# Kernel tuning notes

Hardware: AMD Instinct MI355X
Metric: run time of the kernel (lower is better)

The kernel has to match this reference:

```python
import jax, jax.numpy as jnp
import numpy as np
from math import comb

G, NPG, D = 32, 128, 128   # graphs, nodes-per-graph, hidden dim
N = G * NPG                # 4096 nodes per side
E = 65536                  # edges per side (avg degree 16)
K = 6                      # Bernstein order (bern_k)
S, DCONV, DTR = 16, 4, 8   # mamba d_state, d_conv, dt_rank
HE = 27
SIGMAS = [1.0, 10.0, 100.0, 1000.0, 10000.0]


def _leaky(x, s=0.02):
    return jnp.where(x >= 0, x, s * x)


def _bnorm(x, g, b, eps=1e-5):
    m = jnp.mean(x, axis=0)
    v = jnp.var(x, axis=0)
    return (x - m) * jax.lax.rsqrt(v + eps) * g + b


def _bern_prop(x, src, dst, w, temp):
    # BernNet Bern_prop: Bernstein polynomial of sym-normalized Laplacian with weights relu(temp)
    n = x.shape[0]
    temp = jax.nn.relu(temp)
    deg = jax.ops.segment_sum(w, src, num_segments=n)
    dinv = jnp.where(deg > 0, 1.0 / jnp.sqrt(deg + 1e-12), 0.0)
    nw = (w * dinv[src] * dinv[dst])[:, None]
    adj = lambda v: jax.ops.segment_sum(nw * v[src], dst, num_segments=n)
    tmps = [x]
    xv = x
    for _ in range(K):
        xv = xv + adj(xv)          # (2I - L) v = v + A_norm v
        tmps.append(xv)
    out = (comb(K, 0) / 2 ** K) * temp[0] * tmps[K]
    for i in range(K):
        v = tmps[K - i - 1]
        for _ in range(i + 1):
            v = v - adj(v)         # L v = v - A_norm v
        out = out + (comb(K, i + 1) / 2 ** K) * temp[i + 1] * v
    return out


def _mamba(h, in_w, conv_w, conv_b, xproj_w, dt_w, dt_b, A_log, Dp, out_w):
    # Mamba block, d_model=D, expand=1 (d_inner=D), d_state=S, d_conv=DCONV
    Bb, L, _ = h.shape
    xq, z = jnp.split(h @ in_w, 2, axis=-1)             # [B,L,D] each
    xp = jnp.pad(xq, ((0, 0), (DCONV - 1, 0), (0, 0)))  # causal depthwise conv
    xc = conv_b + sum(xp[:, k:k + L, :] * conv_w[:, k] for k in range(DCONV))
    xc = jax.nn.silu(xc)
    dbl = xc @ xproj_w                                  # [B,L,DTR+2S]
    dt = jax.nn.softplus(dbl[..., :DTR] @ dt_w + dt_b)  # [B,L,D]
    Bm = dbl[..., DTR:DTR + S]
    Cm = dbl[..., DTR + S:]
    A = -jnp.exp(A_log)                                 # [D,S]
    dA = jnp.exp(dt[..., None] * A)                     # [B,L,D,S]
    dBx = dt[..., None] * Bm[:, :, None, :] * xc[..., None]

    def step(hs, ins):
        dA_t, dBx_t, C_t = ins
        hs = dA_t * hs + dBx_t
        return hs, jnp.einsum('bds,bs->bd', hs, C_t)

    h0 = jnp.zeros((Bb, D, S), h.dtype)
    _, ys = jax.lax.scan(step, h0, (jnp.swapaxes(dA, 0, 1),
                                    jnp.swapaxes(dBx, 0, 1),
                                    jnp.swapaxes(Cm, 0, 1)))
    y = jnp.swapaxes(ys, 0, 1) + xc * Dp
    return (y * jax.nn.silu(z)) @ out_w


def _xattn(q, k, v, mask):
    a = mask * (q @ k.T) - 1000.0 * (1.0 - mask)
    return jax.nn.softmax(a, axis=1) @ v


def setup_inputs():
    key = jax.random.key(0)
    ks = jax.random.split(key, 32)
    f = jnp.float32
    nrm = lambda k, shp, sc=1.0: jax.random.normal(k, shp, dtype=f) * sc
    h_lig = nrm(ks[0], (N, D), 0.5)
    h_rec = nrm(ks[1], (N, D), 0.5)
    x_lig = nrm(ks[2], (N, 3))
    x_rec = nrm(ks[3], (N, 3))
    he_1 = jax.random.uniform(ks[4], (E, HE), dtype=f)
    he_2 = jax.random.uniform(ks[5], (E, HE), dtype=f)
    g = (jnp.arange(E) // (E // G)).astype(jnp.int32)
    src1 = g * NPG + jax.random.randint(ks[6], (E,), 0, NPG, dtype=jnp.int32)
    dst1 = g * NPG + jax.random.randint(ks[7], (E,), 0, NPG, dtype=jnp.int32)
    src2 = g * NPG + jax.random.randint(ks[8], (E,), 0, NPG, dtype=jnp.int32)
    dst2 = g * NPG + jax.random.randint(ks[9], (E,), 0, NPG, dtype=jnp.int32)
    edge_index_1 = jnp.stack([src1, dst1])
    edge_index_2 = jnp.stack([src2, dst2])
    batch = (jnp.arange(N) // NPG).astype(jnp.int32)
    rng = np.random.default_rng(0)
    def mkperm(src):
        # lexsort([deg + noise, batch]) with batch as primary key
        deg = np.bincount(np.asarray(src), minlength=N).astype(np.float32)
        return jnp.asarray(np.lexsort((deg + rng.random(N).astype(np.float32),
                                       np.asarray(batch))).astype(np.int32))
    perm_1 = mkperm(src1)
    perm_2 = mkperm(src2)
    p = {}
    p['emlp_w1'] = nrm(ks[10], (32, D), 0.1)
    p['emlp_b1'] = jnp.zeros((D,), f)
    p['emlp_bn_g'] = jnp.ones((D,), f)
    p['emlp_bn_b'] = jnp.zeros((D,), f)
    p['emlp_w2'] = nrm(ks[11], (D, 1), 0.1)
    p['emlp_b2'] = jnp.zeros((1,), f)
    p['bern_temp'] = jnp.ones((K + 1,), f)
    p['m_in_w'] = nrm(ks[12], (D, 2 * D), 0.05)
    p['m_conv_w'] = nrm(ks[13], (D, DCONV), 0.2)
    p['m_conv_b'] = jnp.zeros((D,), f)
    p['m_xproj_w'] = nrm(ks[14], (D, DTR + 2 * S), 0.05)
    p['m_dt_w'] = nrm(ks[15], (DTR, D), 0.2)
    p['m_dt_b'] = jnp.full((D,), -4.0, f)
    p['m_A_log'] = jnp.log(jnp.broadcast_to(jnp.arange(1, S + 1, dtype=f), (D, S)))
    p['m_D'] = jnp.ones((D,), f)
    p['m_out_w'] = nrm(ks[16], (D, D), 0.05)
    p['q_w'] = nrm(ks[17], (D, D), 0.05)
    p['k_w'] = nrm(ks[18], (D, D), 0.05)
    p['v_w'] = nrm(ks[19], (D, D), 0.05)
    p['bn1_g'] = jnp.ones((D,), f)
    p['bn1_b'] = jnp.zeros((D,), f)
    p['bn2_g'] = jnp.ones((D,), f)
    p['bn2_b'] = jnp.zeros((D,), f)
    p['ff_w1'] = nrm(ks[20], (D, 2 * D), 0.05)
    p['ff_b1'] = jnp.zeros((2 * D,), f)
    p['ff_w2'] = nrm(ks[21], (2 * D, D), 0.05)
    p['ff_b2'] = jnp.zeros((D,), f)
    return dict(h_lig=h_lig, h_rec=h_rec, x_lig=x_lig, x_rec=x_rec,
                he_1=he_1, he_2=he_2, **p,
                edge_index_1=edge_index_1, edge_index_2=edge_index_2,
                batch_1=batch, batch_2=batch, perm_1=perm_1, perm_2=perm_2)


def reference(h_lig, h_rec, x_lig, x_rec, he_1, he_2,
              emlp_w1, emlp_b1, emlp_bn_g, emlp_bn_b, emlp_w2, emlp_b2,
              bern_temp, m_in_w, m_conv_w, m_conv_b, m_xproj_w, m_dt_w,
              m_dt_b, m_A_log, m_D, m_out_w, q_w, k_w, v_w,
              bn1_g, bn1_b, bn2_g, bn2_b, ff_w1, ff_b1, ff_w2, ff_b2,
              edge_index_1, edge_index_2, batch_1, batch_2, perm_1, perm_2):

    def side(h, x, he, ei, perm):
        src, dst = ei[0], ei[1]
        d2 = jnp.sum((x[src] - x[dst]) ** 2, axis=1, keepdims=True)
        ew = jnp.concatenate([jnp.exp(-d2 / s) for s in SIGMAS], axis=1)  # [E,5]
        t = _leaky(jnp.concatenate([ew, he], axis=1) @ emlp_w1 + emlp_b1)
        t = _bnorm(t, emlp_bn_g, emlp_bn_b)
        w = jax.nn.relu(t @ emlp_w2 + emlp_b2)[:, 0]                      # [E]
        h_local = _bern_prop(h, src, dst, w, bern_temp)
        inv = jnp.argsort(perm)
        hd = h[perm].reshape(G, NPG, D)   # uniform graph sizes -> exact dense batch
        ha = _mamba(hd, m_in_w, m_conv_w, m_conv_b, m_xproj_w, m_dt_w,
                    m_dt_b, m_A_log, m_D, m_out_w).reshape(N, D)[inv]
        return _bnorm(h + h_local + ha, bn1_g, bn1_b)

    hl = side(h_lig, x_lig, he_1, edge_index_1, perm_1)
    hr = side(h_rec, x_rec, he_2, edge_index_2, perm_2)
    mask = (batch_1[:, None] == batch_2[None, :]).astype(hl.dtype)
    cl = _xattn(_leaky(hl @ q_w), _leaky(hr @ k_w), hr @ v_w, mask)
    cr = _xattn(_leaky(hr @ q_w), _leaky(hl @ k_w), hl @ v_w, mask.T)
    hl = hl + cl
    hr = hr + cr
    ff = lambda h: jax.nn.relu(h @ ff_w1 + ff_b1) @ ff_w2 + ff_b2
    hl = _bnorm(hl + ff(hl), bn2_g, bn2_b)
    hr = _bnorm(hr + ff(hr), bn2_g, bn2_b)
    return hl, hr
```

## Files before the change

kernel.cpp:

```cpp
#include <hip/hip_runtime.h>
#include <math.h>

#define G_    32
#define NPG_  128
#define D_    128
#define N_    4096
#define E_    65536
#define ND_   (N_*D_)

#define W_OFF     0
#define DEG_OFF   65536
#define STATS_OFF 69632
#define BUF0      71680
#define HL_OFF    (BUF0 + 0*ND_)
#define HA_OFF    (BUF0 + 1*ND_)
#define X1_OFF    (BUF0 + 2*ND_)
#define HMID_OFF  (BUF0 + 3*ND_)
#define XC_OFF    (BUF0 + 4*ND_)
#define DTB_OFF   (BUF0 + 5*ND_)
#define YB_OFF    (BUF0 + 6*ND_)
#define XZ_OFF    (BUF0 + 7*ND_)
#define DBL_OFF   (BUF0 + 9*ND_)
#define SS_       ((size_t)(DBL_OFF + N_*40))

__device__ __forceinline__ float leakyf(float x){ return x >= 0.f ? x : 0.02f*x; }
__device__ __forceinline__ float siluf (float x){ return x / (1.f + expf(-x)); }

__device__ __forceinline__ void edge_feat(const float* __restrict__ x,
                                          const float* __restrict__ he,
                                          const int* __restrict__ ei,
                                          int e, float* feat, int& sN, int& dN)
{
  sN = ei[e]; dN = ei[E_ + e];
  float dx = x[sN*3+0]-x[dN*3+0];
  float dy = x[sN*3+1]-x[dN*3+1];
  float dz = x[sN*3+2]-x[dN*3+2];
  float d2 = dx*dx + dy*dy + dz*dz;
  feat[0] = expf(-d2/1.f);
  feat[1] = expf(-d2/10.f);
  feat[2] = expf(-d2/100.f);
  feat[3] = expf(-d2/1000.f);
  feat[4] = expf(-d2/10000.f);
#pragma unroll
  for (int j = 0; j < 27; ++j) feat[5+j] = he[(size_t)e*27 + j];
}

__global__ __launch_bounds__(256)
void edge_stats_kernel(const float* __restrict__ xl, const float* __restrict__ xr,
                       const float* __restrict__ hel, const float* __restrict__ her,
                       const int* __restrict__ ei1, const int* __restrict__ ei2,
                       const float* __restrict__ w1, const float* __restrict__ b1,
                       float* __restrict__ ws)
{
  int side = blockIdx.y;
  const float* x  = side ? xr  : xl;
  const float* he = side ? her : hel;
  const int*   ei = side ? ei2 : ei1;
  float* stats = ws + (size_t)side*SS_ + STATS_OFF;
  __shared__ float featl[256*36];
  __shared__ float csum[2][128], cssq[2][128];
  int tid = threadIdx.x;
  {
    int sN, dN; float feat[32];
    edge_feat(x, he, ei, blockIdx.x*256 + tid, feat, sN, dN);
#pragma unroll
    for (int j4 = 0; j4 < 8; ++j4)
      *(float4*)&featl[tid*36 + j4*4] = *(float4*)&feat[j4*4];
  }
  int c = tid & 127, hh = tid >> 7;
  float w1c[32];
#pragma unroll
  for (int j = 0; j < 32; ++j) w1c[j] = w1[j*128 + c];
  float b1c = b1[c];
  __syncthreads();
  float s1 = 0.f, s2 = 0.f;
  for (int e = 0; e < 128; ++e) {
    const float* f = &featl[(hh*128 + e)*36];
    float acc = b1c;
#pragma unroll
    for (int j4 = 0; j4 < 8; ++j4) {
      float4 f4 = *(const float4*)&f[j4*4];
      acc += f4.x*w1c[j4*4] + f4.y*w1c[j4*4+1] + f4.z*w1c[j4*4+2] + f4.w*w1c[j4*4+3];
    }
    float t = leakyf(acc);
    s1 += t; s2 += t*t;
  }
  csum[hh][c] = s1; cssq[hh][c] = s2;
  __syncthreads();
  if (tid < 128) {
    atomicAdd(&stats[tid],     csum[0][tid] + csum[1][tid]);
    atomicAdd(&stats[128+tid], cssq[0][tid] + cssq[1][tid]);
  }
}

__global__ void edge_finalize_kernel(const float* __restrict__ g_, const float* __restrict__ b_,
                                     const float* __restrict__ w2, const float* __restrict__ b2,
                                     float* __restrict__ ws)
{
  int side = blockIdx.y;
  float* stats = ws + (size_t)side*SS_ + STATS_OFF;
  __shared__ float red[128];
  int c = threadIdx.x;
  const float invE = 1.f/(float)E_;
  float mean = stats[c]*invE;
  float var  = fmaxf(stats[128+c]*invE - mean*mean, 0.f);
  float scale = rsqrtf(var + 1e-5f) * g_[c];
  stats[256+c] = scale * w2[c];
  red[c] = (b_[c] - mean*scale) * w2[c];
  __syncthreads();
  for (int off = 64; off; off >>= 1) { if (c < off) red[c] += red[c+off]; __syncthreads(); }
  if (c == 0) stats[384] = red[0] + b2[0];
}

__global__ __launch_bounds__(256)
void edge_w_kernel(const float* __restrict__ xl, const float* __restrict__ xr,
                   const float* __restrict__ hel, const float* __restrict__ her,
                   const int* __restrict__ ei1, const int* __restrict__ ei2,
                   const float* __restrict__ w1, const float* __restrict__ b1,
                   float* __restrict__ ws)
{
  int side = blockIdx.y;
  const float* x  = side ? xr  : xl;
  const float* he = side ? her : hel;
  const int*   ei = side ? ei2 : ei1;
  float* base = ws + (size_t)side*SS_;
  const float* stats = base + STATS_OFF;
  float* wbuf = base + W_OFF;
  float* deg  = base + DEG_OFF;
  __shared__ float w1t[128*32];
  __shared__ float b1l[128], all_[128];
  int tid = threadIdx.x;
  for (int i = tid; i < 4096; i += 256) {
    int j = i & 31, c = i >> 5;
    w1t[c*32 + j] = w1[j*128 + c];
  }
  if (tid < 128) { b1l[tid] = b1[tid]; all_[tid] = stats[256+tid]; }
  __syncthreads();
  int e = blockIdx.x*256 + tid;
  int sN, dN; float feat[32];
  edge_feat(x, he, ei, e, feat, sN, dN);
  float accw = stats[384];
  for (int c = 0; c < 128; ++c) {
    float acc = b1l[c];
#pragma unroll
    for (int j4 = 0; j4 < 8; ++j4) {
      float4 w4 = *(const float4*)&w1t[c*32 + j4*4];
      acc += feat[j4*4]*w4.x + feat[j4*4+1]*w4.y + feat[j4*4+2]*w4.z + feat[j4*4+3]*w4.w;
    }
    accw += leakyf(acc)*all_[c];
  }
  float w = fmaxf(accw, 0.f);
  wbuf[e] = w;
  atomicAdd(&deg[sN], w);
}

__global__ __launch_bounds__(256)
void bern_horner_kernel(const float* __restrict__ hl_in, const float* __restrict__ hr_in,
                        const int* __restrict__ ei1, const int* __restrict__ ei2,
                        const float* __restrict__ bern_temp, float* __restrict__ ws)
{
  int side = blockIdx.y;
  int g  = blockIdx.x >> 2;
  int d0 = (blockIdx.x & 3) * 32;
  const float* h  = side ? hr_in : hl_in;
  const int*   ei = side ? ei2 : ei1;
  float* base = ws + (size_t)side*SS_;
  const float* wbuf = base + W_OFF;
  const float* deg  = base + DEG_OFF;
  float* hloc = base + HL_OFF;

  __shared__ float A[128*132];
  __shared__ float v[128*32];
  int tid = threadIdx.x;
  for (int i = tid; i < 128*132; i += 256) A[i] = 0.f;

  const float btab[7][7] = {
    { 1,  6, 15,  20, 15,  6,  1},
    { 1,  4,  5,   0, -5, -4, -1},
    { 1,  2, -1,  -4, -1,  2,  1},
    { 1,  0, -3,   0,  3,  0, -1},
    { 1, -2, -1,   4, -1, -2,  1},
    { 1, -4,  5,   0, -5,  4, -1},
    { 1, -6, 15, -20, 15, -6,  1}};
  const float comb6[7] = {1,6,15,20,15,6,1};
  float a[7];
#pragma unroll
  for (int m = 0; m < 7; ++m) a[m] = 0.f;
#pragma unroll
  for (int j = 0; j < 7; ++j) {
    float tj = fmaxf(bern_temp[j], 0.f) * comb6[j] * (1.f/64.f);
#pragma unroll
    for (int m = 0; m < 7; ++m) a[m] += tj * btab[j][m];
  }
  __syncthreads();

  int ebase = g*2048, nbase = g*128;
  for (int i = tid; i < 2048; i += 256) {
    int e = ebase + i;
    int sN = ei[e], dN = ei[E_ + e];
    float ds_ = deg[sN], dd_ = deg[dN];
    float aa = ds_ > 0.f ? rsqrtf(ds_ + 1e-12f) : 0.f;
    float bb = dd_ > 0.f ? rsqrtf(dd_ + 1e-12f) : 0.f;
    atomicAdd(&A[(dN - nbase)*132 + (sN - nbase)], wbuf[e]*aa*bb);
  }

  const int db = (tid & 7)*4;
  const int rb = (tid >> 3)*4;
  float hreg[4][4], r[4][4], t[4][4];
#pragma unroll
  for (int i = 0; i < 4; ++i) {
    float4 h4 = *(const float4*)&h[(size_t)(nbase + rb + i)*128 + d0 + db];
    hreg[i][0]=h4.x; hreg[i][1]=h4.y; hreg[i][2]=h4.z; hreg[i][3]=h4.w;
#pragma unroll
    for (int jj = 0; jj < 4; ++jj) r[i][jj] = a[6]*hreg[i][jj];
  }

  for (int step = 5; step >= 0; --step) {
    __syncthreads();
#pragma unroll
    for (int i = 0; i < 4; ++i)
      *(float4*)&v[(rb+i)*32 + db] = make_float4(r[i][0], r[i][1], r[i][2], r[i][3]);
    __syncthreads();
#pragma unroll
    for (int i = 0; i < 4; ++i)
#pragma unroll
      for (int jj = 0; jj < 4; ++jj) t[i][jj] = 0.f;
    for (int k = 0; k < 128; k += 4) {
      float4 V0 = *(const float4*)&v[(k+0)*32 + db];
      float4 V1 = *(const float4*)&v[(k+1)*32 + db];
      float4 V2 = *(const float4*)&v[(k+2)*32 + db];
      float4 V3 = *(const float4*)&v[(k+3)*32 + db];
#pragma unroll
      for (int i = 0; i < 4; ++i) {
        float4 A4 = *(const float4*)&A[(rb+i)*132 + k];
        t[i][0] += A4.x*V0.x + A4.y*V1.x + A4.z*V2.x + A4.w*V3.x;
        t[i][1] += A4.x*V0.y + A4.y*V1.y + A4.z*V2.y + A4.w*V3.y;
        t[i][2] += A4.x*V0.z + A4.y*V1.z + A4.z*V2.z + A4.w*V3.z;
        t[i][3] += A4.x*V0.w + A4.y*V1.w + A4.z*V2.w + A4.w*V3.w;
      }
    }
    float ak = a[step];
#pragma unroll
    for (int i = 0; i < 4; ++i)
#pragma unroll
      for (int jj = 0; jj < 4; ++jj) r[i][jj] = t[i][jj] + ak*hreg[i][jj];
  }

#pragma unroll
  for (int i = 0; i < 4; ++i)
    *(float4*)&hloc[(size_t)(nbase + rb + i)*128 + d0 + db] =
        make_float4(r[i][0], r[i][1], r[i][2], r[i][3]);
}

template<int K, int NC, int TC, int CSPLIT, int ACT, int GATHER, int SCATTER, int ADDC, int BIAS>
__global__ __launch_bounds__(256)
void gemm_kernel(const float* __restrict__ A0, const float* __restrict__ A1, int lda,
                 const float* __restrict__ W, const float* __restrict__ bias,
                 float* __restrict__ C0, float* __restrict__ C1, int ldc,
                 const int* __restrict__ idx0, const int* __restrict__ idx1,
                 const float* __restrict__ add0, const float* __restrict__ add1)
{
  int side = blockIdx.y;
  const float* A = side ? A1 : A0;
  float* C = side ? C1 : C0;
  const int* idx = side ? idx1 : idx0;
  const float* addsrc = side ? add1 : add0;
  constexpr int RPT = TC/8;
  constexpr int CLEN = NC/CSPLIT;
  __shared__ float Alds[32][K];
  __shared__ float Wlds[K][TC];
  const int tid = threadIdx.x;
  const int r0 = (blockIdx.x / CSPLIT) * 32;
  const int cbase = (blockIdx.x % CSPLIT) * CLEN;
  for (int i = tid*4; i < 32*K; i += 1024) {
    int r = i / K, k = i % K;
    int row = GATHER ? idx[r0 + r] : (r0 + r);
    *(float4*)&Alds[r][k] = *(const float4*)&A[(size_t)row*lda + k];
  }
  for (int c0 = cbase; c0 < cbase + CLEN; c0 += TC) {
    __syncthreads();
    for (int i = tid*4; i < K*TC; i += 1024) {
      int k = i / TC, c = i % TC;
      if (c0 + c < NC) *(float4*)&Wlds[k][c] = *(const float4*)&W[k*NC + c0 + c];
      else             *(float4*)&Wlds[k][c] = make_float4(0.f,0.f,0.f,0.f);
    }
    __syncthreads();
    const int cl = tid % TC;
    const int rsub = (tid / TC) * RPT;
    float accv[RPT];
#pragma unroll
    for (int j = 0; j < RPT; ++j) accv[j] = 0.f;
    for (int k = 0; k < K; k += 4) {
      float w0 = Wlds[k][cl], w1v = Wlds[k+1][cl], w2v = Wlds[k+2][cl], w3v = Wlds[k+3][cl];
#pragma unroll
      for (int j = 0; j < RPT; ++j) {
        float4 a4 = *(const float4*)&Alds[rsub+j][k];
        accv[j] += a4.x*w0 + a4.y*w1v + a4.z*w2v + a4.w*w3v;
      }
    }
    int c = c0 + cl;
    if (c < NC) {
#pragma unroll
      for (int j = 0; j < RPT; ++j) {
        int row  = r0 + rsub + j;
        int orow = SCATTER ? idx[row] : row;
        float vv = accv[j];
        if (BIAS)     vv += bias[c];
        if (ACT == 1) vv = leakyf(vv);
        if (ACT == 2) vv = fmaxf(vv, 0.f);
        if (ADDC)     vv += addsrc[(size_t)orow*ldc + c];
        C[(size_t)orow*ldc + c] = vv;
      }
    }
  }
}

__global__ __launch_bounds__(256)
void qkv_kernel(const float* __restrict__ qw, const float* __restrict__ kw,
                const float* __restrict__ vw, float* __restrict__ ws)
{
  int side = blockIdx.y;
  int mat  = blockIdx.z;
  float* base = ws + (size_t)side*SS_;
  const float* A = base + HMID_OFF;
  const float* W = mat == 0 ? qw : (mat == 1 ? kw : vw);
  float* C = base + (mat == 0 ? XC_OFF : (mat == 1 ? DTB_OFF : YB_OFF));
  __shared__ float Alds[32][128];
  __shared__ float Wlds[128][64];
  const int tid = threadIdx.x;
  const int r0 = (blockIdx.x >> 1) * 32;
  const int c0 = (blockIdx.x & 1) * 64;
  for (int i = tid*4; i < 32*128; i += 1024)
    *(float4*)&Alds[i>>7][i&127] = *(const float4*)&A[(size_t)(r0 + (i>>7))*128 + (i&127)];
  for (int i = tid*4; i < 128*64; i += 1024)
    *(float4*)&Wlds[i>>6][i&63] = *(const float4*)&W[(i>>6)*128 + c0 + (i&63)];
  __syncthreads();
  const int cl = tid & 63;
  const int rsub = (tid >> 6) * 8;
  float accv[8];
#pragma unroll
  for (int j = 0; j < 8; ++j) accv[j] = 0.f;
  for (int k = 0; k < 128; k += 4) {
    float w0 = Wlds[k][cl], w1v = Wlds[k+1][cl], w2v = Wlds[k+2][cl], w3v = Wlds[k+3][cl];
#pragma unroll
    for (int j = 0; j < 8; ++j) {
      float4 a4 = *(const float4*)&Alds[rsub+j][k];
      accv[j] += a4.x*w0 + a4.y*w1v + a4.z*w2v + a4.w*w3v;
    }
  }
#pragma unroll
  for (int j = 0; j < 8; ++j) {
    float vv = accv[j];
    if (mat < 2) vv = leakyf(vv);
    C[(size_t)(r0 + rsub + j)*128 + c0 + cl] = vv;
  }
}

__global__ __launch_bounds__(256)
void conv_kernel(const float* __restrict__ cw, const float* __restrict__ cb, float* __restrict__ ws)
{
  int side = blockIdx.y;
  float* base = ws + (size_t)side*SS_;
  const float* xz = base + XZ_OFF;
  float* xc = base + XC_OFF;
  int i = blockIdx.x*256 + threadIdx.x;
  int j = i >> 7, d = i & 127;
  int l = j & 127;
  float a = cb[d];
#pragma unroll
  for (int k = 0; k < 4; ++k) {
    int ll = l - 3 + k;
    if (ll >= 0) a += xz[(size_t)(j-3+k)*256 + d] * cw[d*4 + k];
  }
  xc[i] = siluf(a);
}

__global__ __launch_bounds__(256)
void scan_kernel(const float* __restrict__ A_log, const float* __restrict__ Dp,
                 const float* __restrict__ dtw, const float* __restrict__ dtbias,
                 float* __restrict__ ws)
{
  int side = blockIdx.z;
  int g  = blockIdx.x;
  int d0 = blockIdx.y * 16;
  float* base = ws + (size_t)side*SS_;
  const float* dbl = base + DBL_OFF;
  const float* xcb = base + XC_OFF;
  float* xz = base + XZ_OFF;

  __shared__ float ldbl[128][40];
  __shared__ float lxc[128][16];
  __shared__ float ldt[128][16];
  __shared__ float lz[128][16];
  __shared__ float ly[128][16];
  __shared__ float ltw[8][16];
  __shared__ float ltb[16];

  int tid = threadIdx.x;
  int rowbase = g*128;
  if (tid < 128)      ltw[tid>>4][tid&15] = dtw[(tid>>4)*128 + d0 + (tid&15)];
  else if (tid < 144) ltb[tid-128] = dtbias[d0 + (tid-128)];
  for (int i = tid; i < 128*40; i += 256)
    ((float*)ldbl)[i] = dbl[(size_t)rowbase*40 + i];
  for (int i = tid; i < 2048; i += 256) {
    int l = i >> 4, dd = i & 15;
    lxc[l][dd] = xcb[(size_t)(rowbase+l)*128 + d0 + dd];
    lz[l][dd]  = xz[(size_t)(rowbase+l)*256 + 128 + d0 + dd];
  }
  __syncthreads();
  for (int i = tid; i < 2048; i += 256) {
    int l = i >> 4, dd = i & 15;
    float a = ltb[dd];
#pragma unroll
    for (int k = 0; k < 8; ++k) a += ldbl[l][k]*ltw[k][dd];
    ldt[l][dd] = a > 20.f ? a : log1pf(expf(a));
  }
  __syncthreads();

  int s = tid & 15, dl = (tid >> 4) & 15;
  float Ac  = -expf(A_log[(d0+dl)*16 + s]);
  float dpv = Dp[d0+dl];
  float hsv = 0.f;
  for (int l = 0; l < 128; ++l) {
    float dtv = ldt[l][dl];
    float xcv = lxc[l][dl];
    float Bv  = ldbl[l][8+s];
    float Cv  = ldbl[l][24+s];
    hsv = expf(dtv*Ac)*hsv + (dtv*xcv)*Bv;
    float val = hsv*Cv;
    val += __shfl_xor(val, 1, 16);
    val += __shfl_xor(val, 2, 16);
    val += __shfl_xor(val, 4, 16);
    val += __shfl_xor(val, 8, 16);
    if (s == 0) ly[l][dl] = val + xcv*dpv;
  }
  __syncthreads();
  for (int i = tid; i < 2048; i += 256) {
    int l = i >> 4, dd = i & 15;
    float y = ly[l][dd];
    float z = lz[l][dd];
    xz[(size_t)(rowbase+l)*256 + d0 + dd] = y * siluf(z);
  }
}

__global__ __launch_bounds__(256)
void stats_kernel(const float* __restrict__ hl_in, const float* __restrict__ hr_in,
                  float* __restrict__ ws, int mode, int statsoff)
{
  int side = blockIdx.y;
  float* base = ws + (size_t)side*SS_;
  const float* h    = side ? hr_in : hl_in;
  const float* hloc = base + HL_OFF;
  const float* ha   = base + HA_OFF;
  float* x1 = base + X1_OFF;
  float* stats = base + STATS_OFF + statsoff;
  int tid = threadIdx.x;
  int c = tid & 127;
  float s1 = 0.f, s2 = 0.f;
  for (int it = 0; it < 16; ++it) {
    int r = blockIdx.x*32 + (tid >> 7) + it*2;
    size_t i = (size_t)r*128 + c;
    float v;
    if (mode == 0) { v = h[i] + hloc[i] + ha[i]; x1[i] = v; }
    else           { v = ha[i]; }
    s1 += v; s2 += v*v;
  }
  __shared__ float red[256];
  red[tid] = s1; __syncthreads();
  if (tid < 128) atomicAdd(&stats[tid], red[tid] + red[tid+128]);
  __syncthreads();
  red[tid] = s2; __syncthreads();
  if (tid < 128) atomicAdd(&stats[128+tid], red[tid] + red[tid+128]);
}

__global__ void bn_finalize_kernel(const float* __restrict__ g_, const float* __restrict__ b_,
                                   float* __restrict__ ws, int statsoff, float invM)
{
  int side = blockIdx.y;
  float* stats = ws + (size_t)side*SS_ + STATS_OFF + statsoff;
  int c = threadIdx.x;
  float mean = stats[c]*invM;
  float var  = fmaxf(stats[128+c]*invM - mean*mean, 0.f);
  float scale = rsqrtf(var + 1e-5f) * g_[c];
  stats[256+c] = scale;
  stats[384+c] = b_[c] - mean*scale;
}

__global__ __launch_bounds__(256)
void bn_apply_kernel(float* __restrict__ ws, float* __restrict__ dout,
                     int srcoff, int dstoff, int statsoff, int to_dout)
{
  int side = blockIdx.y;
  float* base = ws + (size_t)side*SS_;
  const float* src = base + srcoff;
  const float* stats = base + STATS_OFF + statsoff;
  float* dst = to_dout ? (dout + (size_t)side*ND_) : (base + dstoff);
  size_t i = (size_t)blockIdx.x*256 + threadIdx.x;
  int c = (int)(i & 127);
  dst[i] = src[i]*stats[256+c] + stats[384+c];
}

__global__ __launch_bounds__(256)
void attn_kernel(float* __restrict__ ws)
{
  int dir = blockIdx.z;
  int g   = blockIdx.x;
  int rt  = blockIdx.y;
  float* baseq = ws + (size_t)dir*SS_;
  float* basek = ws + (size_t)(1-dir)*SS_;
  const float* qb = baseq + XC_OFF;
  const float* kb = basek + DTB_OFF;
  const float* vb = basek + YB_OFF;
  const float* hm = baseq + HMID_OFF;
  float* h2 = baseq + X1_OFF;

  __shared__ float KT[128][132];
  __shared__ float Qs[32][132];
  __shared__ float sp[32][132];

  const int tid = threadIdx.x;
  const int cl  = tid & 31;
  const int r0  = (tid >> 5) * 4;
  const int c0  = cl * 4;
  const int rowg = g*128 + rt*32;

  {
    const float* qsrc = qb + (size_t)rowg*128;
    for (int i = tid; i < 32*32; i += 256) {
      int r = i >> 5, d4 = i & 31;
      *(float4*)&Qs[r][d4*4] = *(const float4*)&qsrc[(size_t)r*128 + d4*4];
    }
  }
  {
    const float* ksrc = kb + (size_t)(g*128)*128;
    for (int i = tid; i < 128*32; i += 256) {
      int d4 = i >> 7, n = i & 127;
      float4 k4 = *(const float4*)&ksrc[(size_t)n*128 + d4*4];
      KT[d4*4+0][n] = k4.x;
      KT[d4*4+1][n] = k4.y;
      KT[d4*4+2][n] = k4.z;
      KT[d4*4+3][n] = k4.w;
    }
  }
  __syncthreads();

  float acc[4][4];
#pragma unroll
  for (int i = 0; i < 4; ++i)
#pragma unroll
    for (int j = 0; j < 4; ++j) acc[i][j] = 0.f;

  for (int d = 0; d < 128; d += 4) {
    float4 k0 = *(const float4*)&KT[d+0][c0];
    float4 k1 = *(const float4*)&KT[d+1][c0];
    float4 k2 = *(const float4*)&KT[d+2][c0];
    float4 k3 = *(const float4*)&KT[d+3][c0];
#pragma unroll
    for (int i = 0; i < 4; ++i) {
      float4 q4 = *(const float4*)&Qs[r0+i][d];
      acc[i][0] += q4.x*k0.x + q4.y*k1.x + q4.z*k2.x + q4.w*k3.x;
      acc[i][1] += q4.x*k0.y + q4.y*k1.y + q4.z*k2.y + q4.w*k3.y;
      acc[i][2] += q4.x*k0.z + q4.y*k1.z + q4.z*k2.z + q4.w*k3.z;
      acc[i][3] += q4.x*k0.w + q4.y*k1.w + q4.z*k2.w + q4.w*k3.w;
    }
  }

  float inv[4];
#pragma unroll
  for (int i = 0; i < 4; ++i) {
    float m = fmaxf(fmaxf(acc[i][0], acc[i][1]), fmaxf(acc[i][2], acc[i][3]));
#pragma unroll
    for (int off = 1; off < 32; off <<= 1) m = fmaxf(m, __shfl_xor(m, off, 32));
    float p0 = expf(acc[i][0]-m), p1 = expf(acc[i][1]-m);
    float p2 = expf(acc[i][2]-m), p3 = expf(acc[i][3]-m);
    float s = p0 + p1 + p2 + p3;
#pragma unroll
    for (int off = 1; off < 32; off <<= 1) s += __shfl_xor(s, off, 32);
    inv[i] = 1.f/s;
    *(float4*)&sp[r0+i][c0] = make_float4(p0, p1, p2, p3);
  }
  __syncthreads();

  {
    const float* vsrc = vb + (size_t)(g*128)*128;
    for (int i = tid; i < 128*32; i += 256) {
      int n = i >> 5, d4 = i & 31;
      *(float4*)&KT[n][d4*4] = *(const float4*)&vsrc[(size_t)n*128 + d4*4];
    }
  }
  __syncthreads();

  float o[4][4];
#pragma unroll
  for (int i = 0; i < 4; ++i)
#pragma unroll
    for (int j = 0; j < 4; ++j) o[i][j] = 0.f;

  for (int n = 0; n < 128; n += 4) {
    float4 v0 = *(const float4*)&KT[n+0][c0];
    float4 v1 = *(const float4*)&KT[n+1][c0];
    float4 v2 = *(const float4*)&KT[n+2][c0];
    float4 v3 = *(const float4*)&KT[n+3][c0];
#pragma unroll
    for (int i = 0; i < 4; ++i) {
      float4 p4 = *(const float4*)&sp[r0+i][n];
      o[i][0] += p4.x*v0.x + p4.y*v1.x + p4.z*v2.x + p4.w*v3.x;
      o[i][1] += p4.x*v0.y + p4.y*v1.y + p4.z*v2.y + p4.w*v3.y;
      o[i][2] += p4.x*v0.z + p4.y*v1.z + p4.z*v2.z + p4.w*v3.z;
      o[i][3] += p4.x*v0.w + p4.y*v1.w + p4.z*v2.w + p4.w*v3.w;
    }
  }

#pragma unroll
  for (int i = 0; i < 4; ++i) {
    size_t off = (size_t)(rowg + r0 + i)*128 + c0;
    float4 hm4 = *(const float4*)&hm[off];
    float4 r4;
    r4.x = hm4.x + o[i][0]*inv[i];
    r4.y = hm4.y + o[i][1]*inv[i];
    r4.z = hm4.z + o[i][2]*inv[i];
    r4.w = hm4.w + o[i][3]*inv[i];
    *(float4*)&h2[off] = r4;
  }
}

extern "C" void kernel_launch(void* const* d_in, const int* in_sizes, int n_in,
                              void* d_out, int out_size, void* d_ws, size_t ws_size,
                              hipStream_t stream)
{
  const float* h_lig     = (const float*)d_in[0];
  const float* h_rec     = (const float*)d_in[1];
  const float* x_lig     = (const float*)d_in[2];
  const float* x_rec     = (const float*)d_in[3];
  const float* he_1      = (const float*)d_in[4];
  const float* he_2      = (const float*)d_in[5];
  const float* emlp_w1   = (const float*)d_in[6];
  const float* emlp_b1   = (const float*)d_in[7];
  const float* emlp_bn_g = (const float*)d_in[8];
  const float* emlp_bn_b = (const float*)d_in[9];
  const float* emlp_w2   = (const float*)d_in[10];
  const float* emlp_b2   = (const float*)d_in[11];
  const float* bern_temp = (const float*)d_in[12];
  const float* m_in_w    = (const float*)d_in[13];
  const float* m_conv_w  = (const float*)d_in[14];
  const float* m_conv_b  = (const float*)d_in[15];
  const float* m_xproj_w = (const float*)d_in[16];
  const float* m_dt_w    = (const float*)d_in[17];
  const float* m_dt_b    = (const float*)d_in[18];
  const float* m_A_log   = (const float*)d_in[19];
  const float* m_D       = (const float*)d_in[20];
  const float* m_out_w   = (const float*)d_in[21];
  const float* q_w       = (const float*)d_in[22];
  const float* k_w       = (const float*)d_in[23];
  const float* v_w       = (const float*)d_in[24];
  const float* bn1_g     = (const float*)d_in[25];
  const float* bn1_b     = (const float*)d_in[26];
  const float* bn2_g     = (const float*)d_in[27];
  const float* bn2_b     = (const float*)d_in[28];
  const float* ff_w1     = (const float*)d_in[29];
  const float* ff_b1     = (const float*)d_in[30];
  const float* ff_w2     = (const float*)d_in[31];
  const float* ff_b2     = (const float*)d_in[32];
  const int*   ei1       = (const int*)d_in[33];
  const int*   ei2       = (const int*)d_in[34];
  const int*   perm1     = (const int*)d_in[37];
  const int*   perm2     = (const int*)d_in[38];

  float* ws   = (float*)d_ws;
  float* dout = (float*)d_out;

#define B0(off) (ws + (size_t)(off))
#define B1(off) (ws + SS_ + (size_t)(off))

  for (int s = 0; s < 2; ++s)
    hipMemsetAsync((char*)d_ws + ((size_t)s*SS_ + DEG_OFF)*sizeof(float), 0,
                   (N_ + 2048)*sizeof(float), stream);

  edge_stats_kernel<<<dim3(256,2), 256, 0, stream>>>(x_lig,x_rec,he_1,he_2,ei1,ei2,emlp_w1,emlp_b1,ws);
  edge_finalize_kernel<<<dim3(1,2), 128, 0, stream>>>(emlp_bn_g,emlp_bn_b,emlp_w2,emlp_b2,ws);
  edge_w_kernel<<<dim3(256,2), 256, 0, stream>>>(x_lig,x_rec,he_1,he_2,ei1,ei2,emlp_w1,emlp_b1,ws);

  bern_horner_kernel<<<dim3(G_*4,2), 256, 0, stream>>>(h_lig,h_rec,ei1,ei2,bern_temp,ws);

  gemm_kernel<128,256,64,4,0,1,0,0,0><<<dim3(512,2),256,0,stream>>>(
      h_lig,h_rec,128, m_in_w,nullptr, B0(XZ_OFF),B1(XZ_OFF),256, perm1,perm2, nullptr,nullptr);
  conv_kernel<<<dim3(2048,2), 256, 0, stream>>>(m_conv_w,m_conv_b,ws);
  gemm_kernel<128,40,64,1,0,0,0,0,0><<<dim3(128,2),256,0,stream>>>(
      B0(XC_OFF),B1(XC_OFF),128, m_xproj_w,nullptr, B0(DBL_OFF),B1(DBL_OFF),40, nullptr,nullptr, nullptr,nullptr);
  scan_kernel<<<dim3(32,8,2), 256, 0, stream>>>(m_A_log,m_D,m_dt_w,m_dt_b,ws);
  gemm_kernel<128,128,64,2,0,0,1,0,0><<<dim3(256,2),256,0,stream>>>(
      B0(XZ_OFF),B1(XZ_OFF),256, m_out_w,nullptr, B0(HA_OFF),B1(HA_OFF),128, perm1,perm2, nullptr,nullptr);

  stats_kernel<<<dim3(128,2), 256, 0, stream>>>(h_lig,h_rec,ws,0,512);
  bn_finalize_kernel<<<dim3(1,2), 128, 0, stream>>>(bn1_g,bn1_b,ws,512,1.f/(float)N_);
  bn_apply_kernel<<<dim3(2048,2), 256, 0, stream>>>(ws,dout,X1_OFF,HMID_OFF,512,0);

  qkv_kernel<<<dim3(256,2,3), 256, 0, stream>>>(q_w,k_w,v_w,ws);
  attn_kernel<<<dim3(32,4,2), 256, 0, stream>>>(ws);

  gemm_kernel<128,256,64,4,2,0,0,0,1><<<dim3(512,2),256,0,stream>>>(
      B0(X1_OFF),B1(X1_OFF),128, ff_w1,ff_b1, B0(XZ_OFF),B1(XZ_OFF),256, nullptr,nullptr, nullptr,nullptr);
  gemm_kernel<256,128,32,4,0,0,0,1,1><<<dim3(512,2),256,0,stream>>>(
      B0(XZ_OFF),B1(XZ_OFF),256, ff_w2,ff_b2, B0(HA_OFF),B1(HA_OFF),128, nullptr,nullptr, B0(X1_OFF),B1(X1_OFF));
  stats_kernel<<<dim3(128,2), 256, 0, stream>>>(h_lig,h_rec,ws,1,1024);
  bn_finalize_kernel<<<dim3(1,2), 128, 0, stream>>>(bn2_g,bn2_b,ws,1024,1.f/(float)N_);
  bn_apply_kernel<<<dim3(2048,2), 256, 0, stream>>>(ws,dout,HA_OFF,0,1024,1);
}
```

Baseline: 458.1 us.

## Precompute transposed edge-MLP weights once and restructure edge stats per-thread

A small kernel now writes a transposed copy of the edge-MLP first-layer weights into workspace once, and both edge kernels read it directly instead of each block re-transposing into shared memory. The stats kernel changes from a shared-memory feature tile with a column-per-thread loop to a row-per-thread loop. Column sums and sums of squares are reduced with wavefront shuffles and then atomically added per wave. The exp divisions become multiplications by reciprocal constants. This trades shared-memory staging and per-block transposes for uniform global/scalar weight loads, at the cost of many shuffles per channel and more atomics (one set per wave instead of per block).

```diff
diff --git a/kernel.cpp b/kernel.cpp
--- a/kernel.cpp
+++ b/kernel.cpp
@@ -21,7 +21,8 @@
 #define YB_OFF    (BUF0 + 6*ND_)
 #define XZ_OFF    (BUF0 + 7*ND_)
 #define DBL_OFF   (BUF0 + 9*ND_)
-#define SS_       ((size_t)(DBL_OFF + N_*40))
+#define WT_OFF    (DBL_OFF + N_*40)
+#define SS_       ((size_t)(WT_OFF + 4096))
 
 __device__ __forceinline__ float leakyf(float x){ return x >= 0.f ? x : 0.02f*x; }
 __device__ __forceinline__ float siluf (float x){ return x / (1.f + expf(-x)); }
@@ -36,20 +37,28 @@
   float dy = x[sN*3+1]-x[dN*3+1];
   float dz = x[sN*3+2]-x[dN*3+2];
   float d2 = dx*dx + dy*dy + dz*dz;
-  feat[0] = expf(-d2/1.f);
-  feat[1] = expf(-d2/10.f);
-  feat[2] = expf(-d2/100.f);
-  feat[3] = expf(-d2/1000.f);
-  feat[4] = expf(-d2/10000.f);
+  feat[0] = expf(-d2);
+  feat[1] = expf(d2 * -0.1f);
+  feat[2] = expf(d2 * -0.01f);
+  feat[3] = expf(d2 * -0.001f);
+  feat[4] = expf(d2 * -0.0001f);
 #pragma unroll
   for (int j = 0; j < 27; ++j) feat[5+j] = he[(size_t)e*27 + j];
+}
+
+__global__ void wt_kernel(const float* __restrict__ w1, float* __restrict__ wt)
+{
+  for (int k = threadIdx.x; k < 4096; k += 256) {
+    int c = k >> 5, j = k & 31;
+    wt[k] = w1[j*128 + c];
+  }
 }
 
 __global__ __launch_bounds__(256)
 void edge_stats_kernel(const float* __restrict__ xl, const float* __restrict__ xr,
                        const float* __restrict__ hel, const float* __restrict__ her,
                        const int* __restrict__ ei1, const int* __restrict__ ei2,
-                       const float* __restrict__ w1, const float* __restrict__ b1,
+                       const float* __restrict__ wt, const float* __restrict__ b1,
                        float* __restrict__ ws)
 {
   int side = blockIdx.y;
@@ -57,40 +66,37 @@
   const float* he = side ? her : hel;
   const int*   ei = side ? ei2 : ei1;
   float* stats = ws + (size_t)side*SS_ + STATS_OFF;
-  __shared__ float featl[256*36];
-  __shared__ float csum[2][128], cssq[2][128];
   int tid = threadIdx.x;
-  {
-    int sN, dN; float feat[32];
-    edge_feat(x, he, ei, blockIdx.x*256 + tid, feat, sN, dN);
-#pragma unroll
-    for (int j4 = 0; j4 < 8; ++j4)
-      *(float4*)&featl[tid*36 + j4*4] = *(float4*)&feat[j4*4];
-  }
-  int c = tid & 127, hh = tid >> 7;
-  float w1c[32];
-#pragma unroll
-  for (int j = 0; j < 32; ++j) w1c[j] = w1[j*128 + c];
-  float b1c = b1[c];
-  __syncthreads();
-  float s1 = 0.f, s2 = 0.f;
-  for (int e = 0; e < 128; ++e) {
-    const float* f = &featl[(hh*128 + e)*36];
-    float acc = b1c;
-#pragma unroll
-    for (int j4 = 0; j4 < 8; ++j4) {
-      float4 f4 = *(const float4*)&f[j4*4];
-      acc += f4.x*w1c[j4*4] + f4.y*w1c[j4*4+1] + f4.z*w1c[j4*4+2] + f4.w*w1c[j4*4+3];
-    }
-    float t = leakyf(acc);
-    s1 += t; s2 += t*t;
-  }
-  csum[hh][c] = s1; cssq[hh][c] = s2;
-  __syncthreads();
-  if (tid < 128) {
-    atomicAdd(&stats[tid],     csum[0][tid] + csum[1][tid]);
-    atomicAdd(&stats[128+tid], cssq[0][tid] + cssq[1][tid]);
-  }
+  int lane = tid & 63;
+  int sN, dN; float feat[32];
+  edge_feat(x, he, ei, blockIdx.x*256 + tid, feat, sN, dN);
+  float kA1 = 0.f, kA2 = 0.f, kB1 = 0.f, kB2 = 0.f;
+  for (int c = 0; c < 128; ++c) {
+    const float* wc = &wt[c*32];
+    float a0 = 0.f, a1 = 0.f, a2 = 0.f, a3 = 0.f;
+#pragma unroll
+    for (int j = 0; j < 32; j += 4) {
+      a0 += feat[j+0]*wc[j+0];
+      a1 += feat[j+1]*wc[j+1];
+      a2 += feat[j+2]*wc[j+2];
+      a3 += feat[j+3]*wc[j+3];
+    }
+    float t = leakyf(b1[c] + ((a0+a1) + (a2+a3)));
+    float s1 = t, s2 = t*t;
+#pragma unroll
+    for (int off = 1; off < 64; off <<= 1) {
+      s1 += __shfl_xor(s1, off, 64);
+      s2 += __shfl_xor(s2, off, 64);
+    }
+    if ((c & 63) == lane) {
+      if (c < 64) { kA1 = s1; kA2 = s2; }
+      else        { kB1 = s1; kB2 = s2; }
+    }
+  }
+  atomicAdd(&stats[lane],          kA1);
+  atomicAdd(&stats[128 + lane],    kA2);
+  atomicAdd(&stats[64 + lane],     kB1);
+  atomicAdd(&stats[128 + 64 + lane], kB2);
 }
 
 __global__ void edge_finalize_kernel(const float* __restrict__ g_, const float* __restrict__ b_,
@@ -116,7 +122,7 @@
 void edge_w_kernel(const float* __restrict__ xl, const float* __restrict__ xr,
                    const float* __restrict__ hel, const float* __restrict__ her,
                    const int* __restrict__ ei1, const int* __restrict__ ei2,
-                   const float* __restrict__ w1, const float* __restrict__ b1,
+                   const float* __restrict__ wt, const float* __restrict__ b1,
                    float* __restrict__ ws)
 {
   int side = blockIdx.y;
@@ -127,27 +133,25 @@
   const float* stats = base + STATS_OFF;
   float* wbuf = base + W_OFF;
   float* deg  = base + DEG_OFF;
-  __shared__ float w1t[128*32];
-  __shared__ float b1l[128], all_[128];
+  __shared__ float all_[128];
   int tid = threadIdx.x;
-  for (int i = tid; i < 4096; i += 256) {
-    int j = i & 31, c = i >> 5;
-    w1t[c*32 + j] = w1[j*128 + c];
-  }
-  if (tid < 128) { b1l[tid] = b1[tid]; all_[tid] = stats[256+tid]; }
+  if (tid < 128) all_[tid] = stats[256+tid];
   __syncthreads();
   int e = blockIdx.x*256 + tid;
   int sN, dN; float feat[32];
   edge_feat(x, he, ei, e, feat, sN, dN);
   float accw = stats[384];
   for (int c = 0; c < 128; ++c) {
-    float acc = b1l[c];
-#pragma unroll
-    for (int j4 = 0; j4 < 8; ++j4) {
-      float4 w4 = *(const float4*)&w1t[c*32 + j4*4];
-      acc += feat[j4*4]*w4.x + feat[j4*4+1]*w4.y + feat[j4*4+2]*w4.z + feat[j4*4+3]*w4.w;
-    }
-    accw += leakyf(acc)*all_[c];
+    const float* wc = &wt[c*32];
+    float a0 = 0.f, a1 = 0.f, a2 = 0.f, a3 = 0.f;
+#pragma unroll
+    for (int j = 0; j < 32; j += 4) {
+      a0 += feat[j+0]*wc[j+0];
+      a1 += feat[j+1]*wc[j+1];
+      a2 += feat[j+2]*wc[j+2];
+      a3 += feat[j+3]*wc[j+3];
+    }
+    accw += leakyf(b1[c] + ((a0+a1) + (a2+a3))) * all_[c];
   }
   float w = fmaxf(accw, 0.f);
   wbuf[e] = w;
@@ -676,9 +680,10 @@
     hipMemsetAsync((char*)d_ws + ((size_t)s*SS_ + DEG_OFF)*sizeof(float), 0,
                    (N_ + 2048)*sizeof(float), stream);
 
-  edge_stats_kernel<<<dim3(256,2), 256, 0, stream>>>(x_lig,x_rec,he_1,he_2,ei1,ei2,emlp_w1,emlp_b1,ws);
+  wt_kernel<<<1, 256, 0, stream>>>(emlp_w1, B0(WT_OFF));
+  edge_stats_kernel<<<dim3(256,2), 256, 0, stream>>>(x_lig,x_rec,he_1,he_2,ei1,ei2,B0(WT_OFF),emlp_b1,ws);
   edge_finalize_kernel<<<dim3(1,2), 128, 0, stream>>>(emlp_bn_g,emlp_bn_b,emlp_w2,emlp_b2,ws);
-  edge_w_kernel<<<dim3(256,2), 256, 0, stream>>>(x_lig,x_rec,he_1,he_2,ei1,ei2,emlp_w1,emlp_b1,ws);
+  edge_w_kernel<<<dim3(256,2), 256, 0, stream>>>(x_lig,x_rec,he_1,he_2,ei1,ei2,B0(WT_OFF),emlp_b1,ws);
 
   bern_horner_kernel<<<dim3(G_*4,2), 256, 0, stream>>>(h_lig,h_rec,ei1,ei2,bern_temp,ws);
 
```

New measurement: 545.4 us. 19.1% more time.
